# Optimization experiments

Hardware: AMD Instinct MI355X
Metric: run time of the kernel (lower is better)

## Reference

```python
import jax, jax.numpy as jnp
import numpy as np
from jax import lax

C = 256
RED = 16
SK = 7  # spatial kernel


def setup_inputs() -> dict:
    key = jax.random.key(0)
    ks = jax.random.split(key, 12)
    b, c, h, w = 4, C, 64, 64
    cr = c // RED
    c8 = c // 8
    s = lambda fan_in: 1.0 / np.sqrt(fan_in)
    return {
        "x": jax.random.normal(ks[0], (b, c, h, w), dtype=jnp.float32),
        # channel MLP (nn.Linear weights are [out, in], no bias)
        "w1": jax.random.normal(ks[1], (cr, c), dtype=jnp.float32) * s(c),
        "w2": jax.random.normal(ks[2], (c, cr), dtype=jnp.float32) * s(cr),
        # spatial conv: [out=1, in=2, 7, 7], no bias
        "w_sp": jax.random.normal(ks[3], (1, 2, SK, SK), dtype=jnp.float32) * s(2 * SK * SK),
        # 1x1 convs (stored as [out, in]) with bias (Conv2d default bias=True)
        "wq": jax.random.normal(ks[4], (c8, c), dtype=jnp.float32) * s(c),
        "bq": jax.random.normal(ks[5], (c8,), dtype=jnp.float32) * s(c),
        "wk": jax.random.normal(ks[6], (c8, c), dtype=jnp.float32) * s(c),
        "bk": jax.random.normal(ks[7], (c8,), dtype=jnp.float32) * s(c),
        "wv": jax.random.normal(ks[8], (c, c), dtype=jnp.float32) * s(c),
        "bv": jax.random.normal(ks[9], (c,), dtype=jnp.float32) * s(c),
        "gamma": jnp.zeros((1,), dtype=jnp.float32),
    }


def reference(x, w1, w2, w_sp, wq, bq, wk, bk, wv, bv, gamma):
    b, c, h, w = x.shape
    hw = h * w

    # ---- channel attention (CBAM) ----
    avg = jnp.mean(x, axis=(2, 3))          # [b, c]
    mx = jnp.max(x, axis=(2, 3))            # [b, c]
    mlp = lambda v: jax.nn.relu(v @ w1.T) @ w2.T
    ch_att = jax.nn.sigmoid(mlp(avg) + mlp(mx))[:, :, None, None]
    x = x * ch_att

    # ---- spatial attention (CBAM) ----
    avg_s = jnp.mean(x, axis=1, keepdims=True)
    max_s = jnp.max(x, axis=1, keepdims=True)
    sp_in = jnp.concatenate([avg_s, max_s], axis=1)  # [b, 2, h, w]
    pad = SK // 2
    sp = lax.conv_general_dilated(
        sp_in, w_sp, window_strides=(1, 1), padding=[(pad, pad), (pad, pad)],
        dimension_numbers=("NCHW", "OIHW", "NCHW"))
    x = x * jax.nn.sigmoid(sp)

    # ---- non-local self-attention (single head, unscaled) ----
    q = jnp.einsum("bchw,oc->bohw", x, wq) + bq[None, :, None, None]
    k = jnp.einsum("bchw,oc->bohw", x, wk) + bk[None, :, None, None]
    v = jnp.einsum("bchw,oc->bohw", x, wv) + bv[None, :, None, None]
    q = q.reshape(b, -1, hw).transpose(0, 2, 1)   # [b, hw, c/8]
    k = k.reshape(b, -1, hw)                      # [b, c/8, hw]
    v = v.reshape(b, c, hw)                       # [b, c, hw]

    attn = jax.nn.softmax(jnp.einsum("bid,bdj->bij", q, k), axis=-1)  # [b, hw, hw]
    out = jnp.einsum("bcj,bij->bci", v, attn).reshape(b, c, h, w)

    return gamma[0] * out + x
```

## Files before the change

### kernel.cpp

```cpp
#include <hip/hip_runtime.h>
#include <math.h>

constexpr int B_  = 4;
constexpr int C_  = 256;
constexpr int HW_ = 4096;
constexpr int CR_ = 16;
constexpr int CQ_ = 32;
constexpr int NCC = 16;
constexpr int CHK = 16;

__device__ __forceinline__ float sigmoidf_(float x){ return 1.f/(1.f+expf(-x)); }

__global__ void kA(const float* __restrict__ x, float* __restrict__ avg, float* __restrict__ mxv){
  int bc = blockIdx.x;
  const float4* r4 = (const float4*)(x + (size_t)bc*HW_);
  float s = 0.f, m = -INFINITY;
  for (int i = threadIdx.x; i < HW_/4; i += 256){
    float4 v = r4[i];
    s += v.x+v.y+v.z+v.w;
    m = fmaxf(m, fmaxf(fmaxf(v.x,v.y), fmaxf(v.z,v.w)));
  }
  for (int off = 32; off; off >>= 1){
    s += __shfl_down(s, off);
    m = fmaxf(m, __shfl_down(m, off));
  }
  __shared__ float ss[4], sm[4];
  int w = threadIdx.x >> 6, lane = threadIdx.x & 63;
  if (!lane){ ss[w] = s; sm[w] = m; }
  __syncthreads();
  if (!threadIdx.x){
    avg[bc] = (ss[0]+ss[1]+ss[2]+ss[3]) * (1.f/HW_);
    mxv[bc] = fmaxf(fmaxf(sm[0],sm[1]), fmaxf(sm[2],sm[3]));
  }
}

__global__ void kB(const float* __restrict__ avg, const float* __restrict__ mxv,
                   const float* __restrict__ w1, const float* __restrict__ w2,
                   float* __restrict__ att){
  int b = blockIdx.x, t = threadIdx.x;
  __shared__ float sa[C_], sm[C_], hs[CR_];
  sa[t] = avg[b*C_+t]; sm[t] = mxv[b*C_+t];
  __syncthreads();
  if (t < CR_){
    float ha = 0.f, hm = 0.f;
    for (int i = 0; i < C_; i++){ float w = w1[t*C_+i]; ha += w*sa[i]; hm += w*sm[i]; }
    hs[t] = fmaxf(ha, 0.f) + fmaxf(hm, 0.f);
  }
  __syncthreads();
  float o = 0.f;
  for (int h = 0; h < CR_; h++) o += hs[h]*w2[t*CR_+h];
  att[b*C_+t] = sigmoidf_(o);
}

__global__ void kC(const float* __restrict__ x, const float* __restrict__ att,
                   float* __restrict__ psum, float* __restrict__ pmax){
  int bx = blockIdx.x;
  int b = bx >> 6, rem = bx & 63, cc = rem >> 2, tile = rem & 3;
  int t = threadIdx.x;
  __shared__ float satt[CHK];
  if (t < CHK) satt[t] = att[b*C_ + cc*CHK + t];
  __syncthreads();
  int p4 = tile*256 + t;
  const float4* x4 = (const float4*)(x + (size_t)(b*C_ + cc*CHK)*HW_);
  float4 s = {0.f,0.f,0.f,0.f};
  float4 m = {-INFINITY,-INFINITY,-INFINITY,-INFINITY};
  #pragma unroll
  for (int j = 0; j < CHK; j++){
    float a = satt[j];
    float4 v = x4[(size_t)j*(HW_/4) + p4];
    float vx=v.x*a, vy=v.y*a, vz=v.z*a, vw=v.w*a;
    s.x+=vx; s.y+=vy; s.z+=vz; s.w+=vw;
    m.x=fmaxf(m.x,vx); m.y=fmaxf(m.y,vy); m.z=fmaxf(m.z,vz); m.w=fmaxf(m.w,vw);
  }
  ((float4*)psum)[(size_t)(b*NCC+cc)*(HW_/4) + p4] = s;
  ((float4*)pmax)[(size_t)(b*NCC+cc)*(HW_/4) + p4] = m;
}

__global__ void kD(const float* __restrict__ x, const float* __restrict__ att,
                   const float* __restrict__ psum, const float* __restrict__ pmax,
                   const float* __restrict__ wsp, float* __restrict__ out){
  int bx = blockIdx.x;
  int b = bx >> 6, rem = bx & 63, rt = rem >> 2, cp = rem & 3;
  int t = threadIdx.x;
  __shared__ float savg[10][64], smax[10][64], ssig[4][64], satt[64], swsp[98];
  if (t < 98) swsp[t] = wsp[t];
  if (t < 64) satt[t] = att[b*C_ + cp*64 + t];
  for (int idx = t; idx < 640; idx += 256){
    int row = idx >> 6, col = idx & 63;
    int gr = rt*4 - 3 + row;
    float s = 0.f, m = 0.f;
    if ((unsigned)gr < 64u){
      float mm = -INFINITY;
      #pragma unroll
      for (int c2 = 0; c2 < NCC; c2++){
        s  += psum[((b*NCC+c2)<<12) + (gr<<6) + col];
        mm = fmaxf(mm, pmax[((b*NCC+c2)<<12) + (gr<<6) + col]);
      }
      m = mm; s *= (1.f/C_);
    }
    savg[row][col] = s; smax[row][col] = m;
  }
  __syncthreads();
  int trow = t >> 6, col = t & 63;
  float acc = 0.f;
  #pragma unroll
  for (int ky = 0; ky < 7; ky++){
    #pragma unroll
    for (int kx = 0; kx < 7; kx++){
      int gx = col - 3 + kx;
      if ((unsigned)gx < 64u)
        acc += savg[trow+ky][gx]*swsp[ky*7+kx] + smax[trow+ky][gx]*swsp[49+ky*7+kx];
    }
  }
  ssig[trow][col] = sigmoidf_(acc);
  __syncthreads();
  int f4id = t & 63;
  float4 sg4 = ((const float4*)ssig)[f4id];
  int imgo = rt*64 + f4id;
  const float4* x4 = (const float4*)x;
  float4* o4 = (float4*)out;
  #pragma unroll
  for (int jj = 0; jj < 16; jj++){
    int lc = (t>>6) + jj*4;
    float a = satt[lc];
    size_t g = (size_t)(b*C_ + cp*64 + lc)*(HW_/4) + imgo;
    float4 v = x4[g];
    float4 r;
    r.x = v.x*a*sg4.x; r.y = v.y*a*sg4.y; r.z = v.z*a*sg4.z; r.w = v.w*a*sg4.w;
    o4[g] = r;
  }
}

__global__ void kE(const float* __restrict__ gamma, const float* __restrict__ x3,
                   const float* __restrict__ wq, const float* __restrict__ bq,
                   const float* __restrict__ wk, const float* __restrict__ bk,
                   const float* __restrict__ wv, const float* __restrict__ bv,
                   float* __restrict__ qb, float* __restrict__ kb, float* __restrict__ vb){
  if (gamma[0] == 0.f) return;
  int t = threadIdx.x;
  __shared__ float sx[C_*32];
  for (int bx = blockIdx.x; bx < 512; bx += gridDim.x){
    int b = bx >> 7, tile = bx & 127, p0 = tile*32;
    for (int idx = t; idx < C_*32; idx += 256){
      int c = idx >> 5, px = idx & 31;
      sx[idx] = x3[(size_t)(b*C_+c)*HW_ + p0 + px];
    }
    __syncthreads();
    for (int oi = t; oi < CQ_*32; oi += 256){
      int o = oi >> 5, px = oi & 31;
      float aq = bq[o], ak = bk[o];
      for (int c = 0; c < C_; c++){ float xv = sx[c*32+px]; aq += xv*wq[o*C_+c]; ak += xv*wk[o*C_+c]; }
      qb[(size_t)(b*CQ_+o)*HW_ + p0 + px] = aq;
      kb[(size_t)(b*CQ_+o)*HW_ + p0 + px] = ak;
    }
    for (int oi = t; oi < C_*32; oi += 256){
      int o = oi >> 5, px = oi & 31;
      float av = bv[o];
      for (int c = 0; c < C_; c++) av += sx[c*32+px]*wv[o*C_+c];
      vb[(size_t)(b*C_+o)*HW_ + p0 + px] = av;
    }
    __syncthreads();
  }
}

__global__ void kF(const float* __restrict__ gamma, const float* __restrict__ qb,
                   const float* __restrict__ kb, const float* __restrict__ vb,
                   float* __restrict__ ab){
  if (gamma[0] == 0.f) return;
  __shared__ float sq[CQ_];
  __shared__ float sl[HW_];
  __shared__ float red[8];
  int t = threadIdx.x;
  for (int gi = blockIdx.x; gi < B_*HW_; gi += gridDim.x){
    int b = gi >> 12, i = gi & (HW_-1);
    if (t < CQ_) sq[t] = qb[(size_t)(b*CQ_+t)*HW_ + i];
    __syncthreads();
    float lmax = -INFINITY;
    for (int j = t; j < HW_; j += 256){
      float l = 0.f;
      for (int d = 0; d < CQ_; d++) l += sq[d]*kb[(size_t)(b*CQ_+d)*HW_ + j];
      sl[j] = l; lmax = fmaxf(lmax, l);
    }
    for (int off = 32; off; off >>= 1) lmax = fmaxf(lmax, __shfl_down(lmax, off));
    if (!(t & 63)) red[t>>6] = lmax;
    __syncthreads();
    float M = fmaxf(fmaxf(red[0],red[1]), fmaxf(red[2],red[3]));
    float lsum = 0.f;
    for (int j = t; j < HW_; j += 256){ float p = expf(sl[j]-M); sl[j] = p; lsum += p; }
    for (int off = 32; off; off >>= 1) lsum += __shfl_down(lsum, off);
    if (!(t & 63)) red[4+(t>>6)] = lsum;
    __syncthreads();
    float inv = 1.f/(red[4]+red[5]+red[6]+red[7]);
    float acc = 0.f;
    const float* vrow = vb + (size_t)(b*C_+t)*HW_;
    for (int j = 0; j < HW_; j++) acc += sl[j]*vrow[j];
    ab[(size_t)(b*C_+t)*HW_ + i] = acc*inv;
    __syncthreads();
  }
}

__global__ void kG(const float* __restrict__ gamma, const float* __restrict__ ab,
                   float* __restrict__ out){
  float g = gamma[0];
  if (g == 0.f) return;
  size_t n = (size_t)B_*C_*HW_;
  for (size_t i = (size_t)blockIdx.x*256 + threadIdx.x; i < n; i += (size_t)256*gridDim.x)
    out[i] += g*ab[i];
}

extern "C" void kernel_launch(void* const* d_in, const int* in_sizes, int n_in,
                              void* d_out, int out_size, void* d_ws, size_t ws_size,
                              hipStream_t stream){
  const float* x   = (const float*)d_in[0];
  const float* w1  = (const float*)d_in[1];
  const float* w2  = (const float*)d_in[2];
  const float* wsp = (const float*)d_in[3];
  const float* wq  = (const float*)d_in[4];
  const float* bq  = (const float*)d_in[5];
  const float* wk  = (const float*)d_in[6];
  const float* bk  = (const float*)d_in[7];
  const float* wv  = (const float*)d_in[8];
  const float* bv  = (const float*)d_in[9];
  const float* gm  = (const float*)d_in[10];
  float* out = (float*)d_out;
  float* ws  = (float*)d_ws;

  float* avg  = ws;
  float* mxv  = avg  + B_*C_;
  float* att  = mxv  + B_*C_;
  float* psum = att  + B_*C_;
  float* pmax = psum + B_*NCC*HW_;
  float* qb   = pmax + B_*NCC*HW_;
  float* kb   = qb   + B_*CQ_*HW_;
  float* vb   = kb   + B_*CQ_*HW_;
  float* ab   = vb   + (size_t)B_*C_*HW_;
  size_t need_attn = (size_t)((ab + (size_t)B_*C_*HW_) - ws) * sizeof(float);

  kA<<<B_*C_, 256, 0, stream>>>(x, avg, mxv);
  kB<<<B_,    256, 0, stream>>>(avg, mxv, w1, w2, att);
  kC<<<256,   256, 0, stream>>>(x, att, psum, pmax);
  kD<<<256,   256, 0, stream>>>(x, att, psum, pmax, wsp, out);

  if (ws_size >= need_attn){
    kE<<<256, 256, 0, stream>>>(gm, out, wq, bq, wk, bk, wv, bv, qb, kb, vb);
    kF<<<256, 256, 0, stream>>>(gm, qb, kb, vb, ab);
    kG<<<256, 256, 0, stream>>>(gm, ab, out);
  }
}
```

Baseline: 113.8 us.

## Fuse channel MLP into spatial kernels and drop separate gamma-add pass

Removes the standalone channel-MLP kernel by recomputing the MLP redundantly inside each block of the spatial-reduction and apply kernels, using a parallelised 256-thread first layer. The spatial reduction now finishes the full channel reduction inside one block, writing final avg/max maps instead of 16 partials, so the apply kernel reads one value per pixel. The gamma scaling and residual add are folded into the attention kernel, removing the extra elementwise pass. This cuts launches and intermediate traffic in exchange for redundant per-block MLP work; the attention kernels still exit early when gamma is zero.

```diff
diff --git a/kernel.cpp b/kernel.cpp
--- a/kernel.cpp
+++ b/kernel.cpp
@@ -6,10 +6,39 @@
 constexpr int HW_ = 4096;
 constexpr int CR_ = 16;
 constexpr int CQ_ = 32;
-constexpr int NCC = 16;
-constexpr int CHK = 16;
 
 __device__ __forceinline__ float sigmoidf_(float x){ return 1.f/(1.f+expf(-x)); }
+
+__device__ __forceinline__ void ch_att_inline(
+    int b, int t,
+    const float* __restrict__ avg, const float* __restrict__ mxv,
+    const float* __restrict__ w1,  const float* __restrict__ w2,
+    float* sa, float* sm, float* pa, float* pm, float* hs, float* satt){
+  sa[t] = avg[b*C_+t]; sm[t] = mxv[b*C_+t];
+  __syncthreads();
+  int h = t >> 4, seg = t & 15;
+  float qa = 0.f, qm = 0.f;
+  #pragma unroll
+  for (int c2 = 0; c2 < 16; c2++){
+    int c = seg*16 + c2;
+    float w = w1[h*C_ + c];
+    qa += w*sa[c]; qm += w*sm[c];
+  }
+  pa[t] = qa; pm[t] = qm;
+  __syncthreads();
+  if (t < CR_){
+    float ha = 0.f, hm = 0.f;
+    #pragma unroll
+    for (int s = 0; s < 16; s++){ ha += pa[t*16+s]; hm += pm[t*16+s]; }
+    hs[t] = fmaxf(ha, 0.f) + fmaxf(hm, 0.f);
+  }
+  __syncthreads();
+  float o = 0.f;
+  #pragma unroll
+  for (int h2 = 0; h2 < CR_; h2++) o += hs[h2]*w2[t*CR_+h2];
+  satt[t] = sigmoidf_(o);
+  __syncthreads();
+}
 
 __global__ void kA(const float* __restrict__ x, float* __restrict__ avg, float* __restrict__ mxv){
   int bc = blockIdx.x;
@@ -34,69 +63,65 @@
   }
 }
 
-__global__ void kB(const float* __restrict__ avg, const float* __restrict__ mxv,
-                   const float* __restrict__ w1, const float* __restrict__ w2,
-                   float* __restrict__ att){
-  int b = blockIdx.x, t = threadIdx.x;
-  __shared__ float sa[C_], sm[C_], hs[CR_];
-  sa[t] = avg[b*C_+t]; sm[t] = mxv[b*C_+t];
-  __syncthreads();
-  if (t < CR_){
-    float ha = 0.f, hm = 0.f;
-    for (int i = 0; i < C_; i++){ float w = w1[t*C_+i]; ha += w*sa[i]; hm += w*sm[i]; }
-    hs[t] = fmaxf(ha, 0.f) + fmaxf(hm, 0.f);
-  }
-  __syncthreads();
-  float o = 0.f;
-  for (int h = 0; h < CR_; h++) o += hs[h]*w2[t*CR_+h];
-  att[b*C_+t] = sigmoidf_(o);
-}
-
-__global__ void kC(const float* __restrict__ x, const float* __restrict__ att,
-                   float* __restrict__ psum, float* __restrict__ pmax){
-  int bx = blockIdx.x;
-  int b = bx >> 6, rem = bx & 63, cc = rem >> 2, tile = rem & 3;
-  int t = threadIdx.x;
-  __shared__ float satt[CHK];
-  if (t < CHK) satt[t] = att[b*C_ + cc*CHK + t];
-  __syncthreads();
-  int p4 = tile*256 + t;
-  const float4* x4 = (const float4*)(x + (size_t)(b*C_ + cc*CHK)*HW_);
+__global__ void kBC(const float* __restrict__ x,
+                    const float* __restrict__ avg, const float* __restrict__ mxv,
+                    const float* __restrict__ w1,  const float* __restrict__ w2,
+                    float* __restrict__ avgs, float* __restrict__ maxs){
+  int b = blockIdx.x >> 6, r = blockIdx.x & 63, t = threadIdx.x;
+  __shared__ float sa[C_], sm[C_], pa[C_], pm[C_], hs[CR_], satt[C_];
+  __shared__ float4 rs[16][16], rm[16][16];
+  ch_att_inline(b, t, avg, mxv, w1, w2, sa, sm, pa, pm, hs, satt);
+
+  int cg = t >> 4, q = t & 15;
+  const float4* x4 = (const float4*)x;
   float4 s = {0.f,0.f,0.f,0.f};
   float4 m = {-INFINITY,-INFINITY,-INFINITY,-INFINITY};
   #pragma unroll
-  for (int j = 0; j < CHK; j++){
-    float a = satt[j];
-    float4 v = x4[(size_t)j*(HW_/4) + p4];
+  for (int j = 0; j < 16; j++){
+    int c = cg*16 + j;
+    float a = satt[c];
+    float4 v = x4[(size_t)(b*C_+c)*(HW_/4) + (r<<4) + q];
     float vx=v.x*a, vy=v.y*a, vz=v.z*a, vw=v.w*a;
     s.x+=vx; s.y+=vy; s.z+=vz; s.w+=vw;
     m.x=fmaxf(m.x,vx); m.y=fmaxf(m.y,vy); m.z=fmaxf(m.z,vz); m.w=fmaxf(m.w,vw);
   }
-  ((float4*)psum)[(size_t)(b*NCC+cc)*(HW_/4) + p4] = s;
-  ((float4*)pmax)[(size_t)(b*NCC+cc)*(HW_/4) + p4] = m;
-}
-
-__global__ void kD(const float* __restrict__ x, const float* __restrict__ att,
-                   const float* __restrict__ psum, const float* __restrict__ pmax,
-                   const float* __restrict__ wsp, float* __restrict__ out){
+  rs[cg][q] = s; rm[cg][q] = m;
+  __syncthreads();
+  if (t < 16){
+    float4 S = {0.f,0.f,0.f,0.f};
+    float4 M = {-INFINITY,-INFINITY,-INFINITY,-INFINITY};
+    #pragma unroll
+    for (int g = 0; g < 16; g++){
+      float4 a = rs[g][t], b2 = rm[g][t];
+      S.x+=a.x; S.y+=a.y; S.z+=a.z; S.w+=a.w;
+      M.x=fmaxf(M.x,b2.x); M.y=fmaxf(M.y,b2.y); M.z=fmaxf(M.z,b2.z); M.w=fmaxf(M.w,b2.w);
+    }
+    S.x*=(1.f/C_); S.y*=(1.f/C_); S.z*=(1.f/C_); S.w*=(1.f/C_);
+    ((float4*)(avgs + b*HW_ + r*64))[t] = S;
+    ((float4*)(maxs + b*HW_ + r*64))[t] = M;
+  }
+}
+
+__global__ void kD2(const float* __restrict__ x,
+                    const float* __restrict__ avg, const float* __restrict__ mxv,
+                    const float* __restrict__ w1,  const float* __restrict__ w2,
+                    const float* __restrict__ avgs, const float* __restrict__ maxs,
+                    const float* __restrict__ wsp, float* __restrict__ out){
   int bx = blockIdx.x;
   int b = bx >> 6, rem = bx & 63, rt = rem >> 2, cp = rem & 3;
   int t = threadIdx.x;
-  __shared__ float savg[10][64], smax[10][64], ssig[4][64], satt[64], swsp[98];
+  __shared__ float sa[C_], sm[C_], pa[C_], pm[C_], hs[CR_], satt[C_];
+  __shared__ float savg[10][64], smax[10][64], ssig[4][64], swsp[98];
   if (t < 98) swsp[t] = wsp[t];
-  if (t < 64) satt[t] = att[b*C_ + cp*64 + t];
+  ch_att_inline(b, t, avg, mxv, w1, w2, sa, sm, pa, pm, hs, satt);
+
   for (int idx = t; idx < 640; idx += 256){
     int row = idx >> 6, col = idx & 63;
     int gr = rt*4 - 3 + row;
     float s = 0.f, m = 0.f;
     if ((unsigned)gr < 64u){
-      float mm = -INFINITY;
-      #pragma unroll
-      for (int c2 = 0; c2 < NCC; c2++){
-        s  += psum[((b*NCC+c2)<<12) + (gr<<6) + col];
-        mm = fmaxf(mm, pmax[((b*NCC+c2)<<12) + (gr<<6) + col]);
-      }
-      m = mm; s *= (1.f/C_);
+      s = avgs[b*HW_ + gr*64 + col];
+      m = maxs[b*HW_ + gr*64 + col];
     }
     savg[row][col] = s; smax[row][col] = m;
   }
@@ -122,12 +147,12 @@
   #pragma unroll
   for (int jj = 0; jj < 16; jj++){
     int lc = (t>>6) + jj*4;
-    float a = satt[lc];
+    float a = satt[cp*64 + lc];
     size_t g = (size_t)(b*C_ + cp*64 + lc)*(HW_/4) + imgo;
     float4 v = x4[g];
-    float4 r;
-    r.x = v.x*a*sg4.x; r.y = v.y*a*sg4.y; r.z = v.z*a*sg4.z; r.w = v.w*a*sg4.w;
-    o4[g] = r;
+    float4 rr;
+    rr.x = v.x*a*sg4.x; rr.y = v.y*a*sg4.y; rr.z = v.z*a*sg4.z; rr.w = v.w*a*sg4.w;
+    o4[g] = rr;
   }
 }
 
@@ -163,10 +188,11 @@
   }
 }
 
-__global__ void kF(const float* __restrict__ gamma, const float* __restrict__ qb,
-                   const float* __restrict__ kb, const float* __restrict__ vb,
-                   float* __restrict__ ab){
-  if (gamma[0] == 0.f) return;
+__global__ void kF2(const float* __restrict__ gamma, const float* __restrict__ qb,
+                    const float* __restrict__ kb, const float* __restrict__ vb,
+                    float* __restrict__ out){
+  float g = gamma[0];
+  if (g == 0.f) return;
   __shared__ float sq[CQ_];
   __shared__ float sl[HW_];
   __shared__ float red[8];
@@ -190,22 +216,13 @@
     for (int off = 32; off; off >>= 1) lsum += __shfl_down(lsum, off);
     if (!(t & 63)) red[4+(t>>6)] = lsum;
     __syncthreads();
-    float inv = 1.f/(red[4]+red[5]+red[6]+red[7]);
+    float inv = g/(red[4]+red[5]+red[6]+red[7]);
     float acc = 0.f;
     const float* vrow = vb + (size_t)(b*C_+t)*HW_;
     for (int j = 0; j < HW_; j++) acc += sl[j]*vrow[j];
-    ab[(size_t)(b*C_+t)*HW_ + i] = acc*inv;
-    __syncthreads();
-  }
-}
-
-__global__ void kG(const float* __restrict__ gamma, const float* __restrict__ ab,
-                   float* __restrict__ out){
-  float g = gamma[0];
-  if (g == 0.f) return;
-  size_t n = (size_t)B_*C_*HW_;
-  for (size_t i = (size_t)blockIdx.x*256 + threadIdx.x; i < n; i += (size_t)256*gridDim.x)
-    out[i] += g*ab[i];
+    out[(size_t)(b*C_+t)*HW_ + i] += acc*inv;
+    __syncthreads();
+  }
 }
 
 extern "C" void kernel_launch(void* const* d_in, const int* in_sizes, int n_in,
@@ -227,23 +244,19 @@
 
   float* avg  = ws;
   float* mxv  = avg  + B_*C_;
-  float* att  = mxv  + B_*C_;
-  float* psum = att  + B_*C_;
-  float* pmax = psum + B_*NCC*HW_;
-  float* qb   = pmax + B_*NCC*HW_;
+  float* avgs = mxv  + B_*C_;
+  float* maxs = avgs + B_*HW_;
+  float* qb   = maxs + B_*HW_;
   float* kb   = qb   + B_*CQ_*HW_;
   float* vb   = kb   + B_*CQ_*HW_;
-  float* ab   = vb   + (size_t)B_*C_*HW_;
-  size_t need_attn = (size_t)((ab + (size_t)B_*C_*HW_) - ws) * sizeof(float);
-
-  kA<<<B_*C_, 256, 0, stream>>>(x, avg, mxv);
-  kB<<<B_,    256, 0, stream>>>(avg, mxv, w1, w2, att);
-  kC<<<256,   256, 0, stream>>>(x, att, psum, pmax);
-  kD<<<256,   256, 0, stream>>>(x, att, psum, pmax, wsp, out);
+  size_t need_attn = (size_t)((vb + (size_t)B_*C_*HW_) - ws) * sizeof(float);
+
+  kA <<<B_*C_, 256, 0, stream>>>(x, avg, mxv);
+  kBC<<<256,   256, 0, stream>>>(x, avg, mxv, w1, w2, avgs, maxs);
+  kD2<<<256,   256, 0, stream>>>(x, avg, mxv, w1, w2, avgs, maxs, wsp, out);
 
   if (ws_size >= need_attn){
-    kE<<<256, 256, 0, stream>>>(gm, out, wq, bq, wk, bk, wv, bv, qb, kb, vb);
-    kF<<<256, 256, 0, stream>>>(gm, qb, kb, vb, ab);
-    kG<<<256, 256, 0, stream>>>(gm, ab, out);
-  }
-}
+    kE <<<256, 256, 0, stream>>>(gm, out, wq, bq, wk, bk, wv, bv, qb, kb, vb);
+    kF2<<<256, 256, 0, stream>>>(gm, qb, kb, vb, out);
+  }
+}
```

Result: faster. 109.2 us (-4.1%).
